# Performance work log

Measured on AMD Instinct MI355X. Metric: run time of the kernel, lower is better.

## Reference

```python
import jax, jax.numpy as jnp
import numpy as np

ROPE_BASE = 10000.0

def rope_2d(x, h, w):
    # x: (b, h, w, c); 2D RoPE, first half of pair-channels rotated by row angle, second by col angle
    b, _, _, c = x.shape
    k_max = c // 4  # c // (2 * num_spatial_dims)
    theta = 1.0 / (ROPE_BASE ** (jnp.arange(k_max, dtype=jnp.float32) / k_max))  # (k_max,)
    ang_h = jnp.arange(h, dtype=jnp.float32)[:, None] * theta  # (h, k_max)
    ang_w = jnp.arange(w, dtype=jnp.float32)[:, None] * theta  # (w, k_max)
    # angles: (h, w, 2*k_max) = cat([i*theta, j*theta], -1)
    angles = jnp.concatenate([
        jnp.broadcast_to(ang_h[:, None, :], (h, w, k_max)),
        jnp.broadcast_to(ang_w[None, :, :], (h, w, k_max)),
    ], axis=-1)
    cos = jnp.cos(angles)  # (h, w, c//2)
    sin = jnp.sin(angles)
    xr = x[..., 0::2]  # consecutive-pair real parts (b,h,w,c//2)
    xi = x[..., 1::2]
    out_r = xr * cos - xi * sin
    out_i = xr * sin + xi * cos
    return jnp.stack([out_r, out_i], axis=-1).reshape(b, h, w, c)

def linear_attention_fwd(x, h, w, qk_w, qk_b, lepe_w, lepe_b, num_heads=4):
    b, n, c = x.shape
    head_dim = c // num_heads
    qk = x @ qk_w.T + qk_b  # (b, n, 2c)
    q, k = qk[..., :c], qk[..., c:]
    v = x
    q = jax.nn.elu(q) + 1.0
    k = jax.nn.elu(k) + 1.0
    q_rope = rope_2d(q.reshape(b, h, w, c), h, w).reshape(b, n, num_heads, head_dim).transpose(0, 2, 1, 3)
    k_rope = rope_2d(k.reshape(b, h, w, c), h, w).reshape(b, n, num_heads, head_dim).transpose(0, 2, 1, 3)
    qh = q.reshape(b, n, num_heads, head_dim).transpose(0, 2, 1, 3)  # (b,H,n,d)
    kh = k.reshape(b, n, num_heads, head_dim).transpose(0, 2, 1, 3)
    vh = v.reshape(b, n, num_heads, head_dim).transpose(0, 2, 1, 3)
    k_mean = kh.mean(axis=2)  # (b,H,d)
    z = 1.0 / (jnp.einsum('bhnd,bhd->bhn', qh, k_mean) + 1e-6)  # (b,H,n)
    inv_n = 1.0 / n
    kv = jnp.einsum('bhnd,bhne->bhde', k_rope, vh) * inv_n  # (b,H,d,d)
    out = jnp.einsum('bhnd,bhde->bhne', q_rope, kv) * z[..., None]  # (b,H,n,d)
    out = out.transpose(0, 2, 1, 3).reshape(b, n, c)
    # LePE: depthwise 3x3 conv on v in NCHW
    v_img = v.reshape(b, h, w, c).transpose(0, 3, 1, 2)  # (b,c,h,w)
    lepe = jax.lax.conv_general_dilated(
        v_img, lepe_w, window_strides=(1, 1), padding='SAME',
        feature_group_count=c, dimension_numbers=('NCHW', 'OIHW', 'NCHW'))
    lepe = lepe + lepe_b[None, :, None, None]
    out = out + lepe.transpose(0, 2, 3, 1).reshape(b, n, c)
    return out.transpose(0, 2, 1).reshape(b, c, h, w)

def setup_inputs() -> dict:
    key = jax.random.key(0)
    ks = jax.random.split(key, 5)
    b, h, w, c = 16, 128, 128, 64
    n = h * w
    x = jax.random.normal(ks[0], (b, n, c), dtype=jnp.float32)
    qk_w = jax.random.normal(ks[1], (2 * c, c), dtype=jnp.float32) * (1.0 / np.sqrt(c))
    qk_b = jax.random.normal(ks[2], (2 * c,), dtype=jnp.float32) * 0.02
    lepe_w = jax.random.normal(ks[3], (c, 1, 3, 3), dtype=jnp.float32) * (1.0 / 3.0)
    lepe_b = jax.random.normal(ks[4], (c,), dtype=jnp.float32) * 0.02
    return {"x": x, "h": h, "w": w, "qk_w": qk_w, "qk_b": qk_b, "lepe_w": lepe_w, "lepe_b": lepe_b}

def reference(x, h, w, qk_w, qk_b, lepe_w, lepe_b):
    return linear_attention_fwd(x, h, w, qk_w, qk_b, lepe_w, lepe_b, num_heads=4)
```

## Files before the change

kernel.cpp:

```cpp
#include <hip/hip_runtime.h>

#define B_   16
#define C_   64
#define HH   128
#define WW   128
#define NN   (HH*WW)
#define PADB 72
#define PADO 66

typedef short short8 __attribute__((ext_vector_type(8)));
typedef float f32x4  __attribute__((ext_vector_type(4)));

#define NEG_L2_10K_OVER16 (-0.8304820237218406f)

__device__ __forceinline__ float act_elu1(float v) {
    return v > 0.f ? v + 1.f : __expf(v);
}
__device__ __forceinline__ short f2bf(float f) {
    union { float f; unsigned u; } v; v.f = f;
    unsigned r = (v.u + 0x7FFFu + ((v.u >> 16) & 1u)) >> 16;
    return (short)r;
}
__device__ __forceinline__ unsigned cvt2bf(float lo, float hi) {
    unsigned r;
    asm("v_cvt_pk_bf16_f32 %0, %1, %2" : "=v"(r) : "v"(lo), "v"(hi));
    return r;
}

__global__ __launch_bounds__(256, 4) void la_phase1(
    const float* __restrict__ x, const float* __restrict__ qk_w,
    const float* __restrict__ qk_b, float* __restrict__ g_kv,
    float* __restrict__ g_km)
{
    __shared__ __align__(16) char pool[4*64*PADB*2 + 256*4];
    float* kmp = (float*)(pool + 36864);

    const int tid  = threadIdx.x;
    const int w    = tid >> 6;
    const int ln   = tid & 15;
    const int quad = (tid >> 4) & 3;
    const int b    = blockIdx.y;
    const int bx   = blockIdx.x;
    const int nid  = ((bx & 7) << 3) | (bx >> 3);
    const int n_base = nid * 256;
    const float* xb = x + (size_t)b * (size_t)(NN * C_);

    const int srow = tid & 63, scol = (tid >> 6) << 2;
    f32x4 xv[2][4];
    #pragma unroll
    for (int it = 0; it < 4; ++it)
        xv[0][it] = *(const f32x4*)(xb + (size_t)(n_base + srow)*C_ + scol + 16*it);
    short8 aFb[2][2];
    {
        const float* ap = xb + (size_t)(n_base + 16*w + ln)*C_;
        #pragma unroll
        for (int ks = 0; ks < 2; ++ks) {
            f32x4 a0 = *(const f32x4*)(ap + 32*ks + 8*quad);
            f32x4 a1 = *(const f32x4*)(ap + 32*ks + 8*quad + 4);
            union { unsigned u[4]; short8 s; } af;
            af.u[0] = cvt2bf(a0[0], a0[1]); af.u[1] = cvt2bf(a0[2], a0[3]);
            af.u[2] = cvt2bf(a1[0], a1[1]); af.u[3] = cvt2bf(a1[2], a1[3]);
            aFb[0][ks] = af.s;
        }
    }

    short8 bk[2][4];
    #pragma unroll
    for (int ks = 0; ks < 2; ++ks)
        #pragma unroll
        for (int nt = 0; nt < 4; ++nt) {
            const float* wp = qk_w + (64 + 16*nt + ln)*C_ + 32*ks + 8*quad;
            f32x4 w0 = *(const f32x4*)wp, w1 = *(const f32x4*)(wp + 4);
            union { unsigned u[4]; short8 s; } uf;
            uf.u[0] = cvt2bf(w0[0], w0[1]); uf.u[1] = cvt2bf(w0[2], w0[3]);
            uf.u[2] = cvt2bf(w1[0], w1[1]); uf.u[3] = cvt2bf(w1[2], w1[3]);
            bk[ks][nt] = uf.s;
        }
    float biasK[4];
    #pragma unroll
    for (int nt = 0; nt < 4; ++nt) biasK[nt] = qk_b[64 + 16*nt + ln];

    float th[2], rs[2], rc[2];
    #pragma unroll
    for (int i = 0; i < 2; ++i) {
        th[i] = exp2f(NEG_L2_10K_OVER16 * (float)(8*i + (ln >> 1)));
        __sincosf(th[i], &rs[i], &rc[i]);
    }

    f32x4 acc2 = {0.f, 0.f, 0.f, 0.f};
    float kmacc[4] = {0.f, 0.f, 0.f, 0.f};
    const int p_base = 16*w + 4*quad;
    const float sgn = (ln & 1) ? 1.f : -1.f;

    #pragma unroll
    for (int ck = 0; ck < 4; ++ck) {
        const int cur = ck & 1;
        const int n0  = n_base + ck*64;
        short* sXT = (short*)(pool + cur*18432);
        short* sKT = (short*)(pool + cur*18432 + 9216);
        __syncthreads();
        #pragma unroll
        for (int it = 0; it < 4; ++it) {
            int k4 = scol + 16*it;
            unsigned p01 = cvt2bf(xv[cur][it][0], xv[cur][it][1]);
            unsigned p23 = cvt2bf(xv[cur][it][2], xv[cur][it][3]);
            sXT[(k4+0)*PADB + srow] = (short)p01;
            sXT[(k4+1)*PADB + srow] = (short)(p01 >> 16);
            sXT[(k4+2)*PADB + srow] = (short)p23;
            sXT[(k4+3)*PADB + srow] = (short)(p23 >> 16);
        }
        if (ck < 3) {
            #pragma unroll
            for (int it = 0; it < 4; ++it)
                xv[cur^1][it] = *(const f32x4*)(xb + (size_t)(n0 + 64 + srow)*C_ + scol + 16*it);
            const float* ap = xb + (size_t)(n0 + 64 + 16*w + ln)*C_;
            #pragma unroll
            for (int ks = 0; ks < 2; ++ks) {
                f32x4 a0 = *(const f32x4*)(ap + 32*ks + 8*quad);
                f32x4 a1 = *(const f32x4*)(ap + 32*ks + 8*quad + 4);
                union { unsigned u[4]; short8 s; } af;
                af.u[0] = cvt2bf(a0[0], a0[1]); af.u[1] = cvt2bf(a0[2], a0[3]);
                af.u[2] = cvt2bf(a1[0], a1[1]); af.u[3] = cvt2bf(a1[2], a1[3]);
                aFb[cur^1][ks] = af.s;
            }
        }
        f32x4 ak[4];
        #pragma unroll
        for (int nt = 0; nt < 4; ++nt) ak[nt] = (f32x4){0.f,0.f,0.f,0.f};
        #pragma unroll
        for (int ks = 0; ks < 2; ++ks)
            #pragma unroll
            for (int nt = 0; nt < 4; ++nt)
                ak[nt] = __builtin_amdgcn_mfma_f32_16x16x32_bf16(aFb[cur][ks], bk[ks][nt], ak[nt], 0, 0, 0);

        const int yc = n0 >> 7;
        const int x0 = n0 & 127;
        float sy[2], cy[2];
        #pragma unroll
        for (int i = 0; i < 2; ++i) __sincosf((float)yc * th[i], &sy[i], &cy[i]);
        #pragma unroll
        for (int nt = 0; nt < 4; ++nt) {
            float xs = 0.f, xc = 1.f;
            if (nt >= 2)
                __sincosf((float)(x0 + p_base) * th[nt & 1], &xs, &xc);
            #pragma unroll
            for (int r = 0; r < 4; ++r) {
                int p_loc = p_base + r;
                float kval = act_elu1(ak[nt][r] + biasK[nt]);
                kmacc[nt] += kval;
                float P = __shfl_xor(kval, 1);
                float s, c;
                if (nt < 2) { s = sy[nt]; c = cy[nt]; }
                else {
                    s = xs; c = xc;
                    float ns = xs*rc[nt & 1] + xc*rs[nt & 1];
                    float nc = xc*rc[nt & 1] - xs*rs[nt & 1];
                    xs = ns; xc = nc;
                }
                sKT[(16*nt + ln)*PADB + p_loc] = f2bf(kval*c + sgn*P*s);
            }
        }
        __syncthreads();
        #pragma unroll
        for (int ks = 0; ks < 2; ++ks) {
            short8 a  = *(const short8*)(sKT + (16*w + ln)*PADB + 32*ks + 8*quad);
            short8 bf = *(const short8*)(sXT + (16*w + ln)*PADB + 32*ks + 8*quad);
            acc2 = __builtin_amdgcn_mfma_f32_16x16x32_bf16(a, bf, acc2, 0, 0, 0);
        }
    }

    float* kvb = g_kv + b*1024;
    #pragma unroll
    for (int r = 0; r < 4; ++r)
        atomicAdd(kvb + w*256 + (4*quad + r)*16 + ln, acc2[r]);
    #pragma unroll
    for (int nt = 0; nt < 4; ++nt) {
        float v = kmacc[nt];
        v += __shfl_xor(v, 16);
        v += __shfl_xor(v, 32);
        if ((tid & 63) < 16) kmp[w*64 + 16*nt + ln] = v;
    }
    __syncthreads();
    if (tid < 64)
        atomicAdd(g_km + b*64 + tid,
                  kmp[tid] + kmp[64 + tid] + kmp[128 + tid] + kmp[192 + tid]);
}

__global__ __launch_bounds__(256, 4) void la_phase2(
    const float* __restrict__ x, const float* __restrict__ qk_w,
    const float* __restrict__ qk_b, const float* __restrict__ lepe_w,
    const float* __restrict__ lepe_b, const float* __restrict__ g_kv,
    const float* __restrict__ g_km, float* __restrict__ out)
{
    __shared__ __align__(16) char pool[5120 + 9216 + 2304 + 16896];
    short* sKVB = (short*)pool;
    short* sQ   = (short*)(pool + 5120);
    float* sWT  = (float*)(pool + 14336);
    float* sOut = (float*)(pool + 16640);

    const int tid  = threadIdx.x;
    const int w    = tid >> 6;
    const int ln   = tid & 15;
    const int quad = (tid >> 4) & 3;
    const int b    = blockIdx.y;
    const int bx   = blockIdx.x;
    const int n0   = (((bx & 7) << 5) | (bx >> 3)) * 64;
    const float* xb = x + (size_t)b * (size_t)(NN * C_);
    const float inv_n = 1.f / (float)NN;

    for (int idx = tid; idx < 1024; idx += 256) {
        int h = idx >> 8, d = (idx >> 4) & 15, e = idx & 15;
        float v = g_kv[b*1024 + idx] * inv_n;
        int rowb = h*16 + e;
        int kpos  = (h & 1) ? 16 + d : d;
        int kzero = (h & 1) ? d : 16 + d;
        sKVB[rowb*40 + kpos]  = f2bf(v);
        sKVB[rowb*40 + kzero] = 0;
    }
    if (tid < 144) {
        float4 lw = *(const float4*)(lepe_w + tid*4);
        float lwv[4] = {lw.x, lw.y, lw.z, lw.w};
        #pragma unroll
        for (int i = 0; i < 4; ++i) {
            int e = tid*4 + i, ch = e / 9, tap = e - ch*9;
            sWT[tap*64 + ch] = lwv[i];
        }
    }
    __syncthreads();

    short8 wq[2][4];
    #pragma unroll
    for (int ks = 0; ks < 2; ++ks)
        #pragma unroll
        for (int nt = 0; nt < 4; ++nt) {
            const float* wp = qk_w + (16*nt + ln)*C_ + 32*ks + 8*quad;
            f32x4 w0 = *(const f32x4*)wp, w1 = *(const f32x4*)(wp + 4);
            union { unsigned u[4]; short8 s; } uf;
            uf.u[0] = cvt2bf(w0[0], w0[1]); uf.u[1] = cvt2bf(w0[2], w0[3]);
            uf.u[2] = cvt2bf(w1[0], w1[1]); uf.u[3] = cvt2bf(w1[2], w1[3]);
            wq[ks][nt] = uf.s;
        }
    float biasq[4], kmv[4];
    #pragma unroll
    for (int nt = 0; nt < 4; ++nt) {
        biasq[nt] = qk_b[16*nt + ln];
        kmv[nt]   = g_km[b*64 + 16*nt + ln];
    }
    short8 aF[2];
    #pragma unroll
    for (int ks = 0; ks < 2; ++ks) {
        const float* ap = xb + (size_t)(n0 + 16*w + ln)*C_ + 32*ks + 8*quad;
        f32x4 a0 = *(const f32x4*)ap, a1 = *(const f32x4*)(ap + 4);
        union { unsigned u[4]; short8 s; } af;
        af.u[0] = cvt2bf(a0[0], a0[1]);
        af.u[1] = cvt2bf(a0[2], a0[3]);
        af.u[2] = cvt2bf(a1[0], a1[1]);
        af.u[3] = cvt2bf(a1[2], a1[3]);
        aF[ks] = af.s;
    }

    const int cg = tid & 15;
    const int pg = tid >> 4;
    const int p0 = 4*pg;
    const int yy = n0 >> 7, xbase = n0 & 127, gx0 = xbase + p0;
    f32x4 accl[4];
    #pragma unroll
    for (int j = 0; j < 4; ++j) accl[j] = (f32x4){0.f,0.f,0.f,0.f};
    #pragma unroll
    for (int dy = -1; dy <= 1; ++dy) {
        int y2 = yy + dy;
        if ((unsigned)y2 >= HH) continue;
        f32x4 wt0 = *(const f32x4*)(sWT + ((dy+1)*3 + 0)*C_ + 4*cg);
        f32x4 wt1 = *(const f32x4*)(sWT + ((dy+1)*3 + 1)*C_ + 4*cg);
        f32x4 wt2 = *(const f32x4*)(sWT + ((dy+1)*3 + 2)*C_ + 4*cg);
        const float* rp = xb + (size_t)(y2*WW)*C_ + 4*cg;
        f32x4 cb[6];
        #pragma unroll
        for (int jj = 0; jj < 6; ++jj) {
            int col = gx0 - 1 + jj;
            cb[jj] = ((unsigned)col < WW) ? *(const f32x4*)(rp + (size_t)col*C_)
                                          : (f32x4){0.f,0.f,0.f,0.f};
        }
        #pragma unroll
        for (int j = 0; j < 4; ++j)
            accl[j] += cb[j]*wt0 + cb[j+1]*wt1 + cb[j+2]*wt2;
    }
    #pragma unroll
    for (int j = 0; j < 4; ++j)
        #pragma unroll
        for (int i = 0; i < 4; ++i)
            sOut[(4*cg + i)*PADO + p0 + j] = accl[j][i];

    f32x4 aq[4];
    #pragma unroll
    for (int nt = 0; nt < 4; ++nt) aq[nt] = (f32x4){0.f,0.f,0.f,0.f};
    #pragma unroll
    for (int ks = 0; ks < 2; ++ks)
        #pragma unroll
        for (int nt = 0; nt < 4; ++nt)
            aq[nt] = __builtin_amdgcn_mfma_f32_16x16x32_bf16(aF[ks], wq[ks][nt], aq[nt], 0, 0, 0);

    float qv[4][4];
    #pragma unroll
    for (int nt = 0; nt < 4; ++nt)
        #pragma unroll
        for (int r = 0; r < 4; ++r) {
            float q0 = act_elu1(aq[nt][r] + biasq[nt]);
            float dp = q0 * kmv[nt];
            dp += __shfl_xor(dp, 1);
            dp += __shfl_xor(dp, 2);
            dp += __shfl_xor(dp, 4);
            dp += __shfl_xor(dp, 8);
            qv[nt][r] = q0 * __builtin_amdgcn_rcpf(dp * inv_n + 1e-6f);
        }

    float th[2], rs[2], rc[2];
    #pragma unroll
    for (int i = 0; i < 2; ++i) {
        th[i] = exp2f(NEG_L2_10K_OVER16 * (float)(8*i + (ln >> 1)));
        __sincosf(th[i], &rs[i], &rc[i]);
    }
    const int ycoord = n0 >> 7;
    const int x0 = n0 & 127;
    float sy[2], cy[2];
    #pragma unroll
    for (int i = 0; i < 2; ++i) __sincosf((float)ycoord * th[i], &sy[i], &cy[i]);
    const int p_base = 16*w + 4*quad;
    const float sgn = (ln & 1) ? 1.f : -1.f;
    #pragma unroll
    for (int nt = 0; nt < 4; ++nt) {
        float xs = 0.f, xc = 1.f;
        if (nt >= 2)
            __sincosf((float)(x0 + p_base) * th[nt & 1], &xs, &xc);
        #pragma unroll
        for (int r = 0; r < 4; ++r) {
            int p_loc = p_base + r;
            float s, c;
            if (nt < 2) { s = sy[nt]; c = cy[nt]; }
            else {
                s = xs; c = xc;
                float ns = xs*rc[nt & 1] + xc*rs[nt & 1];
                float nc = xc*rc[nt & 1] - xs*rs[nt & 1];
                xs = ns; xc = nc;
            }
            float P = __shfl_xor(qv[nt][r], 1);
            sQ[p_loc*PADB + (16*nt + ln)] = f2bf(qv[nt][r]*c + sgn*P*s);
        }
    }
    __syncthreads();

    f32x4 accq[4];
    #pragma unroll
    for (int h = 0; h < 4; ++h) accq[h] = (f32x4){0.f,0.f,0.f,0.f};
    #pragma unroll
    for (int P2 = 0; P2 < 2; ++P2) {
        short8 a = *(const short8*)(sQ + (16*w + ln)*PADB + 32*P2 + 8*quad);
        #pragma unroll
        for (int hh = 0; hh < 2; ++hh) {
            int h = 2*P2 + hh;
            short8 bf = *(const short8*)(sKVB + (h*16 + ln)*40 + 8*quad);
            accq[h] = __builtin_amdgcn_mfma_f32_16x16x32_bf16(a, bf, accq[h], 0, 0, 0);
        }
    }
    #pragma unroll
    for (int h = 0; h < 4; ++h)
        #pragma unroll
        for (int r = 0; r < 4; ++r)
            sOut[(16*h + ln)*PADO + p_base + r] += accq[h][r];
    __syncthreads();

    const int ch = tid >> 2, sub = tid & 3, pp0 = 16*sub;
    const float lb = lepe_b[ch];
    float* outp = out + (size_t)b*(size_t)(C_*NN) + (size_t)ch*NN + n0 + pp0;
    #pragma unroll
    for (int g = 0; g < 4; ++g) {
        float2 a0 = *(const float2*)(sOut + ch*PADO + pp0 + 4*g);
        float2 a1 = *(const float2*)(sOut + ch*PADO + pp0 + 4*g + 2);
        float4 o4 = { a0.x + lb, a0.y + lb, a1.x + lb, a1.y + lb };
        *(float4*)(outp + 4*g) = o4;
    }
}

extern "C" void kernel_launch(void* const* d_in, const int* in_sizes, int n_in,
                              void* d_out, int out_size, void* d_ws, size_t ws_size,
                              hipStream_t stream) {
    const float* x      = (const float*)d_in[0];
    const float* qk_w   = (const float*)d_in[3];
    const float* qk_b   = (const float*)d_in[4];
    const float* lepe_w = (const float*)d_in[5];
    const float* lepe_b = (const float*)d_in[6];
    float* out = (float*)d_out;

    float* g_kv = (float*)d_ws;
    float* g_km = g_kv + 16*1024;
    hipMemsetAsync(d_ws, 0, (size_t)(16*1024 + 16*64) * sizeof(float), stream);

    hipLaunchKernelGGL(la_phase1, dim3(64, B_), dim3(256), 0, stream,
                       x, qk_w, qk_b, g_kv, g_km);
    hipLaunchKernelGGL(la_phase2, dim3(256, B_), dim3(256), 0, stream,
                       x, qk_w, qk_b, lepe_w, lepe_b, g_kv, g_km, out);
}
```

Before: 225.3 us.

## Transpose Q MFMA, alias LDS buffers, use hardware sincos, raise phase2 occupancy

Phase 2 now computes the Q projection with swapped MFMA operands, so each lane holds consecutive channel pairs. That lets RoPE be applied locally without lane shuffles, and the z-normalisation reduction needs only two shuffles. The sQ/sKVB region is aliased with sOut to shrink shared memory, and launch bounds are raised to 8 blocks per CU. An extra barrier is added, and the LePE result is now accumulated after the attention output. Sin/cos are switched to the hardware v_sin/v_cos instructions on revolution-normalised angles, which may slightly change accuracy and adds register pressure under the tighter bound.

```diff
diff --git a/kernel.cpp b/kernel.cpp
--- a/kernel.cpp
+++ b/kernel.cpp
@@ -10,8 +10,10 @@
 
 typedef short short8 __attribute__((ext_vector_type(8)));
 typedef float f32x4  __attribute__((ext_vector_type(4)));
+typedef unsigned uint2v __attribute__((ext_vector_type(2)));
 
 #define NEG_L2_10K_OVER16 (-0.8304820237218406f)
+#define INV2PI 0.15915494309189535f
 
 __device__ __forceinline__ float act_elu1(float v) {
     return v > 0.f ? v + 1.f : __expf(v);
@@ -25,6 +27,11 @@
     unsigned r;
     asm("v_cvt_pk_bf16_f32 %0, %1, %2" : "=v"(r) : "v"(lo), "v"(hi));
     return r;
+}
+__device__ __forceinline__ void hw_sincos(float rev, float* s, float* c) {
+    float f = rev - floorf(rev);
+    *s = __builtin_amdgcn_sinf(f);
+    *c = __builtin_amdgcn_cosf(f);
 }
 
 __global__ __launch_bounds__(256, 4) void la_phase1(
@@ -83,8 +90,8 @@
     float th[2], rs[2], rc[2];
     #pragma unroll
     for (int i = 0; i < 2; ++i) {
-        th[i] = exp2f(NEG_L2_10K_OVER16 * (float)(8*i + (ln >> 1)));
-        __sincosf(th[i], &rs[i], &rc[i]);
+        th[i] = exp2f(NEG_L2_10K_OVER16 * (float)(8*i + (ln >> 1))) * INV2PI;
+        hw_sincos(th[i], &rs[i], &rc[i]);
     }
 
     f32x4 acc2 = {0.f, 0.f, 0.f, 0.f};
@@ -137,12 +144,12 @@
         const int x0 = n0 & 127;
         float sy[2], cy[2];
         #pragma unroll
-        for (int i = 0; i < 2; ++i) __sincosf((float)yc * th[i], &sy[i], &cy[i]);
+        for (int i = 0; i < 2; ++i) hw_sincos((float)yc * th[i], &sy[i], &cy[i]);
         #pragma unroll
         for (int nt = 0; nt < 4; ++nt) {
             float xs = 0.f, xc = 1.f;
             if (nt >= 2)
-                __sincosf((float)(x0 + p_base) * th[nt & 1], &xs, &xc);
+                hw_sincos((float)(x0 + p_base) * th[nt & 1], &xs, &xc);
             #pragma unroll
             for (int r = 0; r < 4; ++r) {
                 int p_loc = p_base + r;
@@ -186,17 +193,17 @@
                   kmp[tid] + kmp[64 + tid] + kmp[128 + tid] + kmp[192 + tid]);
 }
 
-__global__ __launch_bounds__(256, 4) void la_phase2(
+__global__ __launch_bounds__(256, 8) void la_phase2(
     const float* __restrict__ x, const float* __restrict__ qk_w,
     const float* __restrict__ qk_b, const float* __restrict__ lepe_w,
     const float* __restrict__ lepe_b, const float* __restrict__ g_kv,
     const float* __restrict__ g_km, float* __restrict__ out)
 {
-    __shared__ __align__(16) char pool[5120 + 9216 + 2304 + 16896];
+    __shared__ __align__(16) char pool[16896 + 2304];
     short* sKVB = (short*)pool;
     short* sQ   = (short*)(pool + 5120);
-    float* sWT  = (float*)(pool + 14336);
-    float* sOut = (float*)(pool + 16640);
+    float* sOut = (float*)pool;
+    float* sWT  = (float*)(pool + 16896);
 
     const int tid  = threadIdx.x;
     const int w    = tid >> 6;
@@ -226,7 +233,6 @@
             sWT[tap*64 + ch] = lwv[i];
         }
     }
-    __syncthreads();
 
     short8 wq[2][4];
     #pragma unroll
@@ -240,12 +246,6 @@
             uf.u[2] = cvt2bf(w1[0], w1[1]); uf.u[3] = cvt2bf(w1[2], w1[3]);
             wq[ks][nt] = uf.s;
         }
-    float biasq[4], kmv[4];
-    #pragma unroll
-    for (int nt = 0; nt < 4; ++nt) {
-        biasq[nt] = qk_b[16*nt + ln];
-        kmv[nt]   = g_km[b*64 + 16*nt + ln];
-    }
     short8 aF[2];
     #pragma unroll
     for (int ks = 0; ks < 2; ++ks) {
@@ -258,6 +258,72 @@
         af.u[3] = cvt2bf(a1[2], a1[3]);
         aF[ks] = af.s;
     }
+    f32x4 aq[4];
+    #pragma unroll
+    for (int nt = 0; nt < 4; ++nt) aq[nt] = (f32x4){0.f,0.f,0.f,0.f};
+    #pragma unroll
+    for (int ks = 0; ks < 2; ++ks)
+        #pragma unroll
+        for (int nt = 0; nt < 4; ++nt)
+            aq[nt] = __builtin_amdgcn_mfma_f32_16x16x32_bf16(wq[ks][nt], aF[ks], aq[nt], 0, 0, 0);
+
+    float thA[2], thB[2];
+    #pragma unroll
+    for (int s = 0; s < 2; ++s) {
+        thA[s] = exp2f(NEG_L2_10K_OVER16 * (float)(2*quad + s)) * INV2PI;
+        thB[s] = exp2f(NEG_L2_10K_OVER16 * (float)(8 + 2*quad + s)) * INV2PI;
+    }
+    const float ycf = (float)(n0 >> 7);
+    const float xcf = (float)((n0 & 127) + 16*w + ln);
+
+    #pragma unroll
+    for (int nt = 0; nt < 4; ++nt) {
+        f32x4 bq = *(const f32x4*)(qk_b + 16*nt + 4*quad);
+        f32x4 km = *(const f32x4*)(g_km + b*64 + 16*nt + 4*quad);
+        float qv[4], dp = 0.f;
+        #pragma unroll
+        for (int r = 0; r < 4; ++r) {
+            qv[r] = act_elu1(aq[nt][r] + bq[r]);
+            dp += qv[r] * km[r];
+        }
+        dp += __shfl_xor(dp, 16);
+        dp += __shfl_xor(dp, 32);
+        float z = __builtin_amdgcn_rcpf(dp * inv_n + 1e-6f);
+        float coord = (nt < 2) ? ycf : xcf;
+        uint2v pk;
+        #pragma unroll
+        for (int s = 0; s < 2; ++s) {
+            float thv = (nt & 1) ? thB[s] : thA[s];
+            float sn, cs;
+            hw_sincos(coord * thv, &sn, &cs);
+            float e = qv[2*s], o = qv[2*s+1];
+            pk[s] = cvt2bf((e*cs - o*sn) * z, (e*sn + o*cs) * z);
+        }
+        *(uint2v*)(sQ + (16*w + ln)*PADB + 16*nt + 4*quad) = pk;
+    }
+    __syncthreads();
+
+    f32x4 accq[4];
+    #pragma unroll
+    for (int h = 0; h < 4; ++h) accq[h] = (f32x4){0.f,0.f,0.f,0.f};
+    #pragma unroll
+    for (int P2 = 0; P2 < 2; ++P2) {
+        short8 a = *(const short8*)(sQ + (16*w + ln)*PADB + 32*P2 + 8*quad);
+        #pragma unroll
+        for (int hh = 0; hh < 2; ++hh) {
+            int h = 2*P2 + hh;
+            short8 bf = *(const short8*)(sKVB + (h*16 + ln)*40 + 8*quad);
+            accq[h] = __builtin_amdgcn_mfma_f32_16x16x32_bf16(a, bf, accq[h], 0, 0, 0);
+        }
+    }
+    __syncthreads();
+
+    const int p_base = 16*w + 4*quad;
+    #pragma unroll
+    for (int h = 0; h < 4; ++h)
+        #pragma unroll
+        for (int r = 0; r < 4; ++r)
+            sOut[(16*h + ln)*PADO + p_base + r] = accq[h][r];
 
     const int cg = tid & 15;
     const int pg = tid >> 4;
@@ -285,88 +351,12 @@
         for (int j = 0; j < 4; ++j)
             accl[j] += cb[j]*wt0 + cb[j+1]*wt1 + cb[j+2]*wt2;
     }
+    __syncthreads();
     #pragma unroll
     for (int j = 0; j < 4; ++j)
         #pragma unroll
         for (int i = 0; i < 4; ++i)
-            sOut[(4*cg + i)*PADO + p0 + j] = accl[j][i];
-
-    f32x4 aq[4];
-    #pragma unroll
-    for (int nt = 0; nt < 4; ++nt) aq[nt] = (f32x4){0.f,0.f,0.f,0.f};
-    #pragma unroll
-    for (int ks = 0; ks < 2; ++ks)
-        #pragma unroll
-        for (int nt = 0; nt < 4; ++nt)
-            aq[nt] = __builtin_amdgcn_mfma_f32_16x16x32_bf16(aF[ks], wq[ks][nt], aq[nt], 0, 0, 0);
-
-    float qv[4][4];
-    #pragma unroll
-    for (int nt = 0; nt < 4; ++nt)
-        #pragma unroll
-        for (int r = 0; r < 4; ++r) {
-            float q0 = act_elu1(aq[nt][r] + biasq[nt]);
-            float dp = q0 * kmv[nt];
-            dp += __shfl_xor(dp, 1);
-            dp += __shfl_xor(dp, 2);
-            dp += __shfl_xor(dp, 4);
-            dp += __shfl_xor(dp, 8);
-            qv[nt][r] = q0 * __builtin_amdgcn_rcpf(dp * inv_n + 1e-6f);
-        }
-
-    float th[2], rs[2], rc[2];
-    #pragma unroll
-    for (int i = 0; i < 2; ++i) {
-        th[i] = exp2f(NEG_L2_10K_OVER16 * (float)(8*i + (ln >> 1)));
-        __sincosf(th[i], &rs[i], &rc[i]);
-    }
-    const int ycoord = n0 >> 7;
-    const int x0 = n0 & 127;
-    float sy[2], cy[2];
-    #pragma unroll
-    for (int i = 0; i < 2; ++i) __sincosf((float)ycoord * th[i], &sy[i], &cy[i]);
-    const int p_base = 16*w + 4*quad;
-    const float sgn = (ln & 1) ? 1.f : -1.f;
-    #pragma unroll
-    for (int nt = 0; nt < 4; ++nt) {
-        float xs = 0.f, xc = 1.f;
-        if (nt >= 2)
-            __sincosf((float)(x0 + p_base) * th[nt & 1], &xs, &xc);
-        #pragma unroll
-        for (int r = 0; r < 4; ++r) {
-            int p_loc = p_base + r;
-            float s, c;
-            if (nt < 2) { s = sy[nt]; c = cy[nt]; }
-            else {
-                s = xs; c = xc;
-                float ns = xs*rc[nt & 1] + xc*rs[nt & 1];
-                float nc = xc*rc[nt & 1] - xs*rs[nt & 1];
-                xs = ns; xc = nc;
-            }
-            float P = __shfl_xor(qv[nt][r], 1);
-            sQ[p_loc*PADB + (16*nt + ln)] = f2bf(qv[nt][r]*c + sgn*P*s);
-        }
-    }
-    __syncthreads();
-
-    f32x4 accq[4];
-    #pragma unroll
-    for (int h = 0; h < 4; ++h) accq[h] = (f32x4){0.f,0.f,0.f,0.f};
-    #pragma unroll
-    for (int P2 = 0; P2 < 2; ++P2) {
-        short8 a = *(const short8*)(sQ + (16*w + ln)*PADB + 32*P2 + 8*quad);
-        #pragma unroll
-        for (int hh = 0; hh < 2; ++hh) {
-            int h = 2*P2 + hh;
-            short8 bf = *(const short8*)(sKVB + (h*16 + ln)*40 + 8*quad);
-            accq[h] = __builtin_amdgcn_mfma_f32_16x16x32_bf16(a, bf, accq[h], 0, 0, 0);
-        }
-    }
-    #pragma unroll
-    for (int h = 0; h < 4; ++h)
-        #pragma unroll
-        for (int r = 0; r < 4; ++r)
-            sOut[(16*h + ln)*PADO + p_base + r] += accq[h][r];
+            sOut[(4*cg + i)*PADO + p0 + j] += accl[j][i];
     __syncthreads();
 
     const int ch = tid >> 2, sub = tid & 3, pp0 = 16*sub;
```

Result: no change. 226.8 us (+0.7%).
